# Kernel tuning notes

Measured on AMD Instinct MI355X. Metric: run time of the kernel, lower is better.

The kernel has to match this reference:

```python
import jax, jax.numpy as jnp
import numpy as np

N_EMBD = 512
N_HEAD = 8


def setup_inputs() -> dict:
    key = jax.random.key(0)
    k_x, k_aw, k_ab, k_pw, k_pb = jax.random.split(key, 5)
    B, T, E = 4, 2048, N_EMBD
    s = 1.0 / np.sqrt(E)
    return {
        "x": jax.random.normal(k_x, (B, T, E), dtype=jnp.float32),
        # torch Linear weight is [out, in]; store transposed for x @ W
        "c_attn_w": jax.random.uniform(k_aw, (E, 3 * E), jnp.float32, -s, s),
        "c_attn_b": jax.random.uniform(k_ab, (3 * E,), jnp.float32, -s, s),
        "c_proj_w": jax.random.uniform(k_pw, (E, E), jnp.float32, -s, s),
        "c_proj_b": jax.random.uniform(k_pb, (E,), jnp.float32, -s, s),
    }


def reference(x, c_attn_w, c_attn_b, c_proj_w, c_proj_b):
    B, T, E = x.shape
    H = N_HEAD
    D = E // H
    qkv = x @ c_attn_w + c_attn_b                      # [B,T,3E]
    q, k, v = jnp.split(qkv, 3, axis=2)
    # [B,T,E] -> [B,H,T,D]
    q = q.reshape(B, T, H, D).transpose(0, 2, 1, 3)
    k = k.reshape(B, T, H, D).transpose(0, 2, 1, 3)
    v = v.reshape(B, T, H, D).transpose(0, 2, 1, 3)
    scale = 1.0 / np.sqrt(D).astype(np.float32)
    scores = jnp.einsum("bhqd,bhkd->bhqk", q, k) * scale
    causal = jnp.tril(jnp.ones((T, T), dtype=bool))    # [T,T]
    scores = jnp.where(causal, scores, -jnp.inf)
    attn = jax.nn.softmax(scores, axis=-1)             # [B,H,T,T]
    y = jnp.einsum("bhqk,bhkd->bhqd", attn, v)         # [B,H,T,D]
    y = y.transpose(0, 2, 1, 3).reshape(B, T, E)
    return y @ c_proj_w + c_proj_b
```

## Files before the change

kernel.cpp:

```cpp
#include <hip/hip_runtime.h>
#include <math.h>

#define N_EMBD 512
#define N_HEAD 8
#define SEQ_T  2048
#define BATCH  4
#define QKV_LD 1536

typedef __attribute__((ext_vector_type(8))) short bf16x8;
typedef __attribute__((ext_vector_type(4))) float f32x4;

#define CL 0.18033688f

__device__ __forceinline__ unsigned short f2bf(float f) {
    union { float f; unsigned int u; } x; x.f = f;
    return (unsigned short)((x.u + 0x7FFFu + ((x.u >> 16) & 1u)) >> 16);
}
__device__ __forceinline__ unsigned pack_trunc(float a, float b) {
    union { float f; unsigned u; } x, y; x.f = a; y.f = b;
    return __builtin_amdgcn_perm(y.u, x.u, 0x07060302u);
}
__device__ __forceinline__ bf16x8 scale_frag(bf16x8 v, float c) {
    bf16x8 r;
    #pragma unroll
    for (int i = 0; i < 8; ++i) {
        union { unsigned u; float f; } x;
        x.u = ((unsigned)(unsigned short)v[i]) << 16;
        r[i] = (short)f2bf(x.f * c);
    }
    return r;
}

__device__ __forceinline__ void gl_lds16(const void* g, void* s) {
    __builtin_amdgcn_global_load_lds(
        (const __attribute__((address_space(1))) void*)g,
        (__attribute__((address_space(3))) void*)s, 16, 0, 0);
}

__global__ __launch_bounds__(256) void prep(
    const float* __restrict__ x,  unsigned short* __restrict__ x_bf,
    const float* __restrict__ w1, unsigned short* __restrict__ w1t,
    const float* __restrict__ w2, unsigned short* __restrict__ w2t)
{
    __shared__ float t[32][33];
    const int bx = blockIdx.x, tid = threadIdx.x;
    if (bx < 2048) {
        const int i = bx * 256 + tid;
        const float4 a = ((const float4*)x)[i * 2 + 0];
        const float4 b = ((const float4*)x)[i * 2 + 1];
        union { unsigned short u[8]; uint4 v; } r;
        r.u[0]=f2bf(a.x); r.u[1]=f2bf(a.y); r.u[2]=f2bf(a.z); r.u[3]=f2bf(a.w);
        r.u[4]=f2bf(b.x); r.u[5]=f2bf(b.y); r.u[6]=f2bf(b.z); r.u[7]=f2bf(b.w);
        ((uint4*)x_bf)[i] = r.v;
        return;
    }
    const float* W; unsigned short* Wt; int N, tt;
    if (bx < 2816) { tt = bx - 2048; W = w1; Wt = w1t; N = 1536; }
    else           { tt = bx - 2816; W = w2; Wt = w2t; N = 512; }
    const int nb = (bx < 2816) ? 48 : 16;
    const int n0 = (tt % nb) * 32, k0 = (tt / nb) * 32;
    const int tx = tid & 31, ty = tid >> 5;
    #pragma unroll
    for (int i = 0; i < 4; ++i)
        t[ty + i * 8][tx] = W[(size_t)(k0 + ty + i * 8) * N + n0 + tx];
    __syncthreads();
    #pragma unroll
    for (int i = 0; i < 4; ++i)
        Wt[(size_t)(n0 + ty + i * 8) * 512 + k0 + tx] = f2bf(t[tx][ty + i * 8]);
}

template <int BM, int BN, bool BF16_OUT>
__global__ __launch_bounds__(256) void gemm_mfma(
    const unsigned short* __restrict__ A,
    const unsigned short* __restrict__ Bt,
    const float* __restrict__ bias,
    void* __restrict__ C, int N, int K)
{
    constexpr int WMT = BM / 32, WNT = BN / 32;
    constexpr int NIT_A = BM / 64, NIT_B = BN / 64;
    __shared__ unsigned short As[2][BM * 32];
    __shared__ unsigned short Bs[2][BN * 32];

    const int tid  = threadIdx.x;
    const int wave = tid >> 6, lane = tid & 63;
    const int low  = lane & 15, quad = lane >> 4;
    const int wm   = (wave & 1) * (BM / 2), wn = (wave >> 1) * (BN / 2);
    const int row0 = blockIdx.y * BM, col0 = blockIdx.x * BN;

    const unsigned short* pa[NIT_A]; int da[NIT_A];
    #pragma unroll
    for (int i = 0; i < NIT_A; ++i) {
        const int p = wave * BM + i * 64 + lane;
        const int m = p >> 2, o = p & 3;
        const int q = o ^ ((m >> 1) & 3);
        pa[i] = A + (size_t)(row0 + m) * K + q * 8;
        da[i] = (wave * BM + i * 64) * 8;
    }
    const unsigned short* pb[NIT_B]; int db[NIT_B];
    #pragma unroll
    for (int i = 0; i < NIT_B; ++i) {
        const int p = wave * BN + i * 64 + lane;
        const int m = p >> 2, o = p & 3;
        const int q = o ^ ((m >> 1) & 3);
        pb[i] = Bt + (size_t)(col0 + m) * K + q * 8;
        db[i] = (wave * BN + i * 64) * 8;
    }

    f32x4 acc[WMT][WNT];
    #pragma unroll
    for (int i = 0; i < WMT; ++i)
        #pragma unroll
        for (int j = 0; j < WNT; ++j) acc[i][j] = (f32x4){0.f, 0.f, 0.f, 0.f};

    #pragma unroll
    for (int i = 0; i < NIT_A; ++i) gl_lds16(pa[i], &As[0][da[i]]);
    #pragma unroll
    for (int i = 0; i < NIT_B; ++i) gl_lds16(pb[i], &Bs[0][db[i]]);
    __syncthreads();

    const int NIT = K >> 5;
    for (int it = 0; it < NIT; ++it) {
        const int cur = it & 1;
        if (it + 1 < NIT) {
            const int ko = (it + 1) * 32;
            #pragma unroll
            for (int i = 0; i < NIT_A; ++i) gl_lds16(pa[i] + ko, &As[cur ^ 1][da[i]]);
            #pragma unroll
            for (int i = 0; i < NIT_B; ++i) gl_lds16(pb[i] + ko, &Bs[cur ^ 1][db[i]]);
        }
        const int swz = (low >> 1) & 3;
        bf16x8 af[WMT], bfr[WNT];
        #pragma unroll
        for (int t = 0; t < WMT; ++t)
            af[t] = *(const bf16x8*)&As[cur][(wm + t * 16 + low) * 32 + ((quad ^ swz) * 8)];
        #pragma unroll
        for (int t = 0; t < WNT; ++t)
            bfr[t] = *(const bf16x8*)&Bs[cur][(wn + t * 16 + low) * 32 + ((quad ^ swz) * 8)];
        #pragma unroll
        for (int i = 0; i < WMT; ++i)
            #pragma unroll
            for (int j = 0; j < WNT; ++j)
                acc[i][j] = __builtin_amdgcn_mfma_f32_16x16x32_bf16(
                    af[i], bfr[j], acc[i][j], 0, 0, 0);
        __syncthreads();
    }

    float bv[WNT];
    #pragma unroll
    for (int j = 0; j < WNT; ++j) bv[j] = bias[col0 + wn + j * 16 + low];
    #pragma unroll
    for (int i = 0; i < WMT; ++i)
        #pragma unroll
        for (int r = 0; r < 4; ++r) {
            const size_t row = row0 + wm + i * 16 + quad * 4 + r;
            #pragma unroll
            for (int j = 0; j < WNT; ++j) {
                const int col = col0 + wn + j * 16 + low;
                const float v = acc[i][j][r] + bv[j];
                if (BF16_OUT)
                    ((unsigned short*)C)[row * N + col] = f2bf(v);
                else
                    ((float*)C)[row * N + col] = v;
            }
        }
}

template <bool MASK>
__device__ __forceinline__ void tile_step(
    const bf16x8 kf[4][2], const bf16x8 qf0, const bf16x8 qf1,
    int thr, int quad, int low, unsigned short* ps)
{
    f32x4 s[4];
    #pragma unroll
    for (int st = 0; st < 4; ++st) {
        f32x4 a = (f32x4){0.f, 0.f, 0.f, 0.f};
        a = __builtin_amdgcn_mfma_f32_16x16x32_bf16(kf[st][0], qf0, a, 0, 0, 0);
        a = __builtin_amdgcn_mfma_f32_16x16x32_bf16(kf[st][1], qf1, a, 0, 0, 0);
        s[st] = a;
    }
    #pragma unroll
    for (int st = 0; st < 4; ++st) {
        float p[4];
        #pragma unroll
        for (int r = 0; r < 4; ++r) {
            float v = s[st][r];
            if (MASK) v = (st * 16 + r <= thr) ? v : -1e30f;
            p[r] = __builtin_amdgcn_exp2f(v);
        }
        uint2 pk;
        pk.x = pack_trunc(p[0], p[1]);
        pk.y = pack_trunc(p[2], p[3]);
        *(uint2*)&ps[low * 72 + st * 16 + quad * 4] = pk;
    }
}

__device__ __forceinline__ void pv_step(
    const bf16x8 vf[4][2], const unsigned short* ps, int quad, int low,
    f32x4* o, f32x4& lacc, const bf16x8 ones)
{
    const bf16x8 p0 = *(const bf16x8*)&ps[low * 72 + quad * 8];
    const bf16x8 p1 = *(const bf16x8*)&ps[low * 72 + quad * 8 + 32];
    #pragma unroll
    for (int t = 0; t < 4; ++t) {
        o[t] = __builtin_amdgcn_mfma_f32_16x16x32_bf16(p0, vf[t][0], o[t], 0, 0, 0);
        o[t] = __builtin_amdgcn_mfma_f32_16x16x32_bf16(p1, vf[t][1], o[t], 0, 0, 0);
    }
    lacc = __builtin_amdgcn_mfma_f32_16x16x32_bf16(p0, ones, lacc, 0, 0, 0);
    lacc = __builtin_amdgcn_mfma_f32_16x16x32_bf16(p1, ones, lacc, 0, 0, 0);
}

__global__ __launch_bounds__(256) void attn_mfma(
    const unsigned short* __restrict__ qkv,
    unsigned short* __restrict__ y)
{
    const int bh  = blockIdx.y;
    const int b   = bh >> 3, h = bh & 7;
    const int pa  = blockIdx.x;
    const int qA0 = pa * 64;
    const int qB0 = (31 - pa) * 64;
    const int nA  = pa + 1, nB = 32 - pa;
    const int tid = threadIdx.x;
    const int wave = tid >> 6, lane = tid & 63;
    const int low  = lane & 15, quad = lane >> 4;

    __shared__ unsigned short Ks[2][64 * 64];
    __shared__ unsigned short Vt[2][64 * 64];
    __shared__ unsigned short PsA[4][16 * 72];
    __shared__ unsigned short PsB[4][16 * 72];

    const size_t base = (size_t)b * SEQ_T * QKV_LD + h * 64;
    const unsigned short* qp = qkv + base;
    const unsigned short* kp = qkv + base + 512;
    const unsigned short* vp = qkv + base + 1024;

    const int qmyA = qA0 + wave * 16 + low;
    const int qmyB = qB0 + wave * 16 + low;

    const bf16x8 qfA0 = scale_frag(*(const bf16x8*)(qp + (size_t)qmyA * QKV_LD + quad * 8), CL);
    const bf16x8 qfA1 = scale_frag(*(const bf16x8*)(qp + (size_t)qmyA * QKV_LD + quad * 8 + 32), CL);
    const bf16x8 qfB0 = scale_frag(*(const bf16x8*)(qp + (size_t)qmyB * QKV_LD + quad * 8), CL);
    const bf16x8 qfB1 = scale_frag(*(const bf16x8*)(qp + (size_t)qmyB * QKV_LD + quad * 8 + 32), CL);

    bf16x8 ones;
    #pragma unroll
    for (int i = 0; i < 8; ++i) ones[i] = (short)0x3F80;

    const int d0 = wave * 8;
    unsigned short* psA = &PsA[wave][0];
    unsigned short* psB = &PsB[wave][0];

    bf16x8 vr0 = *(const bf16x8*)(vp + (size_t)lane * QKV_LD + d0);
    bf16x8 vr1 = *(const bf16x8*)(vp + (size_t)lane * QKV_LD + d0 + 32);
    {
        #pragma unroll
        for (int ii = 0; ii < 2; ++ii) {
            const int row = wave * 16 + ii * 8 + (lane >> 3);
            const int o   = (lane & 7) ^ (lane >> 3);
            gl_lds16(kp + (size_t)row * QKV_LD + o * 8, &Ks[0][(wave * 2 + ii) * 512]);
        }
        #pragma unroll
        for (int ii = 0; ii < 8; ++ii) {
            const int po = ((lane >> 3) ^ ii) * 8 + (lane & 7);
            Vt[0][((d0 + ii) << 6) + po]      = (unsigned short)vr0[ii];
            Vt[0][((d0 + 32 + ii) << 6) + po] = (unsigned short)vr1[ii];
        }
        if (nB > 1) {
            vr0 = *(const bf16x8*)(vp + (size_t)(64 + lane) * QKV_LD + d0);
            vr1 = *(const bf16x8*)(vp + (size_t)(64 + lane) * QKV_LD + d0 + 32);
        }
    }
    __syncthreads();

    f32x4 oA[4], oB[4], lA, lB;
    #pragma unroll
    for (int t = 0; t < 4; ++t) {
        oA[t] = (f32x4){0.f, 0.f, 0.f, 0.f};
        oB[t] = (f32x4){0.f, 0.f, 0.f, 0.f};
    }
    lA = (f32x4){0.f, 0.f, 0.f, 0.f};
    lB = (f32x4){0.f, 0.f, 0.f, 0.f};

    for (int kc = 0; kc < nB; ++kc) {
        const int cur = kc & 1;
        unsigned short* ksc = &Ks[cur][0];
        unsigned short* vtc = &Vt[cur][0];

        if (kc + 1 < nB) {
            const int key1 = (kc + 1) * 64;
            #pragma unroll
            for (int ii = 0; ii < 2; ++ii) {
                const int row = wave * 16 + ii * 8 + (lane >> 3);
                const int o   = (lane & 7) ^ (lane >> 3);
                gl_lds16(kp + (size_t)(key1 + row) * QKV_LD + o * 8,
                         &Ks[cur ^ 1][(wave * 2 + ii) * 512]);
            }
            unsigned short* vtn = &Vt[cur ^ 1][0];
            #pragma unroll
            for (int ii = 0; ii < 8; ++ii) {
                const int po = ((lane >> 3) ^ ii) * 8 + (lane & 7);
                vtn[((d0 + ii) << 6) + po]      = (unsigned short)vr0[ii];
                vtn[((d0 + 32 + ii) << 6) + po] = (unsigned short)vr1[ii];
            }
        }
        if (kc + 2 < nB) {
            const int key2 = (kc + 2) * 64;
            vr0 = *(const bf16x8*)(vp + (size_t)(key2 + lane) * QKV_LD + d0);
            vr1 = *(const bf16x8*)(vp + (size_t)(key2 + lane) * QKV_LD + d0 + 32);
        }

        const int key0 = kc * 64;
        bf16x8 kf[4][2];
        #pragma unroll
        for (int t = 0; t < 4; ++t)
            #pragma unroll
            for (int i = 0; i < 2; ++i)
                kf[t][i] = *(const bf16x8*)
                    &ksc[((t * 16 + low) << 6) + (((quad + 4 * i) ^ (low & 7)) << 3)];

        if (kc < nA) {
            if (kc == nA - 1)
                tile_step<true >(kf, qfA0, qfA1, qmyA - key0 - quad * 4, quad, low, psA);
            else
                tile_step<false>(kf, qfA0, qfA1, 0, quad, low, psA);
        }
        if (kc == nB - 1)
            tile_step<true >(kf, qfB0, qfB1, qmyB - key0 - quad * 4, quad, low, psB);
        else
            tile_step<false>(kf, qfB0, qfB1, 0, quad, low, psB);

        asm volatile("" ::: "memory");

        bf16x8 vf[4][2];
        #pragma unroll
        for (int t = 0; t < 4; ++t)
            #pragma unroll
            for (int i = 0; i < 2; ++i)
                vf[t][i] = *(const bf16x8*)
                    &vtc[((t * 16 + low) << 6) + (((quad + 4 * i) ^ (low & 7)) << 3)];

        if (kc < nA) pv_step(vf, psA, quad, low, oA, lA, ones);
        pv_step(vf, psB, quad, low, oB, lB, ones);
        __syncthreads();
    }

    #pragma unroll
    for (int r = 0; r < 4; ++r) {
        const float rlA = 1.f / lA[r];
        const int qrow = qA0 + wave * 16 + quad * 4 + r;
        unsigned short* yp = y + (size_t)(b * SEQ_T + qrow) * N_EMBD + h * 64 + low;
        #pragma unroll
        for (int t = 0; t < 4; ++t) yp[16 * t] = f2bf(oA[t][r] * rlA);
    }
    #pragma unroll
    for (int r = 0; r < 4; ++r) {
        const float rlB = 1.f / lB[r];
        const int qrow = qB0 + wave * 16 + quad * 4 + r;
        unsigned short* yp = y + (size_t)(b * SEQ_T + qrow) * N_EMBD + h * 64 + low;
        #pragma unroll
        for (int t = 0; t < 4; ++t) yp[16 * t] = f2bf(oB[t][r] * rlB);
    }
}

extern "C" void kernel_launch(void* const* d_in, const int* in_sizes, int n_in,
                              void* d_out, int out_size, void* d_ws, size_t ws_size,
                              hipStream_t stream)
{
    const float* x      = (const float*)d_in[0];
    const float* attn_w = (const float*)d_in[1];
    const float* attn_b = (const float*)d_in[2];
    const float* proj_w = (const float*)d_in[3];
    const float* proj_b = (const float*)d_in[4];
    float*       out    = (float*)d_out;

    char* ws = (char*)d_ws;
    unsigned short* qkv_bf = (unsigned short*)(ws);
    unsigned short* y_bf   = (unsigned short*)(ws + 25165824);
    unsigned short* x_bf   = (unsigned short*)(ws + 33554432);
    unsigned short* w1t    = (unsigned short*)(ws + 41943040);
    unsigned short* w2t    = (unsigned short*)(ws + 43515904);

    prep<<<3072, 256, 0, stream>>>(x, x_bf, attn_w, w1t, proj_w, w2t);

    gemm_mfma<128, 128, true><<<dim3(12, 64), 256, 0, stream>>>(
        x_bf, w1t, attn_b, qkv_bf, QKV_LD, N_EMBD);

    attn_mfma<<<dim3(16, BATCH * N_HEAD), 256, 0, stream>>>(qkv_bf, y_bf);

    gemm_mfma<64, 128, false><<<dim3(4, 128), 256, 0, stream>>>(
        y_bf, w2t, proj_b, out, N_EMBD, N_EMBD);
}
```

Before: 158.5 us.

## Restructure causal attention into flat work-item stream with register-prefetched K/V

The attention kernel drops the shared-key loop, where the A and B query tiles both consume each K/V chunk. It now runs a flat list of 33 work items (A chunks then B chunks), each a single QK/PV tile. Work items are processed two per iteration, with K and V prefetched into registers two items ahead and stored to padded LDS (72-element K rows instead of swizzling). This gives a uniform per-item cost and overlaps global loads with compute. The trade-off is that K/V chunks shared by A and B are now loaded twice, and the larger Ps buffer uses more LDS. The GEMM loop also moves its barrier to the top of each iteration.

```diff
diff --git a/kernel.cpp b/kernel.cpp
--- a/kernel.cpp
+++ b/kernel.cpp
@@ -116,11 +116,11 @@
     for (int i = 0; i < NIT_A; ++i) gl_lds16(pa[i], &As[0][da[i]]);
     #pragma unroll
     for (int i = 0; i < NIT_B; ++i) gl_lds16(pb[i], &Bs[0][db[i]]);
-    __syncthreads();
 
     const int NIT = K >> 5;
     for (int it = 0; it < NIT; ++it) {
         const int cur = it & 1;
+        __syncthreads();
         if (it + 1 < NIT) {
             const int ko = (it + 1) * 32;
             #pragma unroll
@@ -142,7 +142,6 @@
             for (int j = 0; j < WNT; ++j)
                 acc[i][j] = __builtin_amdgcn_mfma_f32_16x16x32_bf16(
                     af[i], bfr[j], acc[i][j], 0, 0, 0);
-        __syncthreads();
     }
 
     float bv[WNT];
@@ -209,6 +208,30 @@
     lacc = __builtin_amdgcn_mfma_f32_16x16x32_bf16(p1, ones, lacc, 0, 0, 0);
 }
 
+template <bool MASK>
+__device__ __forceinline__ void do_item(
+    const unsigned short* ksb, const unsigned short* vtb, unsigned short* ps,
+    const bf16x8 qf0, const bf16x8 qf1, int thr, int quad, int low,
+    f32x4 (&o)[4], f32x4& l, const bf16x8 ones)
+{
+    bf16x8 kf[4][2];
+    #pragma unroll
+    for (int t = 0; t < 4; ++t)
+        #pragma unroll
+        for (int i = 0; i < 2; ++i)
+            kf[t][i] = *(const bf16x8*)&ksb[(t * 16 + low) * 72 + (quad + 4 * i) * 8];
+    tile_step<MASK>(kf, qf0, qf1, thr, quad, low, ps);
+    asm volatile("" ::: "memory");
+    bf16x8 vf[4][2];
+    #pragma unroll
+    for (int t = 0; t < 4; ++t)
+        #pragma unroll
+        for (int i = 0; i < 2; ++i)
+            vf[t][i] = *(const bf16x8*)
+                &vtb[((t * 16 + low) << 6) + (((quad + 4 * i) ^ (low & 7)) << 3)];
+    pv_step(vf, ps, quad, low, o, l, ones);
+}
+
 __global__ __launch_bounds__(256) void attn_mfma(
     const unsigned short* __restrict__ qkv,
     unsigned short* __restrict__ y)
@@ -218,15 +241,14 @@
     const int pa  = blockIdx.x;
     const int qA0 = pa * 64;
     const int qB0 = (31 - pa) * 64;
-    const int nA  = pa + 1, nB = 32 - pa;
+    const int nA  = pa + 1;
     const int tid = threadIdx.x;
     const int wave = tid >> 6, lane = tid & 63;
     const int low  = lane & 15, quad = lane >> 4;
 
-    __shared__ unsigned short Ks[2][64 * 64];
+    __shared__ unsigned short Ks[2][64 * 72];
     __shared__ unsigned short Vt[2][64 * 64];
-    __shared__ unsigned short PsA[4][16 * 72];
-    __shared__ unsigned short PsB[4][16 * 72];
+    __shared__ unsigned short Ps[2][4][16 * 72];
 
     const size_t base = (size_t)b * SEQ_T * QKV_LD + h * 64;
     const unsigned short* qp = qkv + base;
@@ -245,32 +267,6 @@
     #pragma unroll
     for (int i = 0; i < 8; ++i) ones[i] = (short)0x3F80;
 
-    const int d0 = wave * 8;
-    unsigned short* psA = &PsA[wave][0];
-    unsigned short* psB = &PsB[wave][0];
-
-    bf16x8 vr0 = *(const bf16x8*)(vp + (size_t)lane * QKV_LD + d0);
-    bf16x8 vr1 = *(const bf16x8*)(vp + (size_t)lane * QKV_LD + d0 + 32);
-    {
-        #pragma unroll
-        for (int ii = 0; ii < 2; ++ii) {
-            const int row = wave * 16 + ii * 8 + (lane >> 3);
-            const int o   = (lane & 7) ^ (lane >> 3);
-            gl_lds16(kp + (size_t)row * QKV_LD + o * 8, &Ks[0][(wave * 2 + ii) * 512]);
-        }
-        #pragma unroll
-        for (int ii = 0; ii < 8; ++ii) {
-            const int po = ((lane >> 3) ^ ii) * 8 + (lane & 7);
-            Vt[0][((d0 + ii) << 6) + po]      = (unsigned short)vr0[ii];
-            Vt[0][((d0 + 32 + ii) << 6) + po] = (unsigned short)vr1[ii];
-        }
-        if (nB > 1) {
-            vr0 = *(const bf16x8*)(vp + (size_t)(64 + lane) * QKV_LD + d0);
-            vr1 = *(const bf16x8*)(vp + (size_t)(64 + lane) * QKV_LD + d0 + 32);
-        }
-    }
-    __syncthreads();
-
     f32x4 oA[4], oB[4], lA, lB;
     #pragma unroll
     for (int t = 0; t < 4; ++t) {
@@ -280,68 +276,93 @@
     lA = (f32x4){0.f, 0.f, 0.f, 0.f};
     lB = (f32x4){0.f, 0.f, 0.f, 0.f};
 
-    for (int kc = 0; kc < nB; ++kc) {
-        const int cur = kc & 1;
-        unsigned short* ksc = &Ks[cur][0];
-        unsigned short* vtc = &Vt[cur][0];
-
-        if (kc + 1 < nB) {
-            const int key1 = (kc + 1) * 64;
-            #pragma unroll
-            for (int ii = 0; ii < 2; ++ii) {
-                const int row = wave * 16 + ii * 8 + (lane >> 3);
-                const int o   = (lane & 7) ^ (lane >> 3);
-                gl_lds16(kp + (size_t)(key1 + row) * QKV_LD + o * 8,
-                         &Ks[cur ^ 1][(wave * 2 + ii) * 512]);
-            }
-            unsigned short* vtn = &Vt[cur ^ 1][0];
+    #define ITEM_KC(g) (((g) < nA) ? (g) : ((g) - nA))
+
+    bf16x8 k0a, k0b, v0a, v0b, k1a, k1b, v1a, v1b;
+    {
+        const size_t r0 = (size_t)(ITEM_KC(0) * 64 + lane) * QKV_LD;
+        k0a = *(const bf16x8*)(kp + r0 + wave * 16);
+        k0b = *(const bf16x8*)(kp + r0 + wave * 16 + 8);
+        v0a = *(const bf16x8*)(vp + r0 + wave * 8);
+        v0b = *(const bf16x8*)(vp + r0 + wave * 8 + 32);
+        const size_t r1 = (size_t)(ITEM_KC(1) * 64 + lane) * QKV_LD;
+        k1a = *(const bf16x8*)(kp + r1 + wave * 16);
+        k1b = *(const bf16x8*)(kp + r1 + wave * 16 + 8);
+        v1a = *(const bf16x8*)(vp + r1 + wave * 8);
+        v1b = *(const bf16x8*)(vp + r1 + wave * 8 + 32);
+    }
+
+    const int d0 = wave * 8;
+    for (int i = 0; i < 17; ++i) {
+        const int g0 = 2 * i, g1 = 2 * i + 1;
+
+        __syncthreads();
+
+        *(bf16x8*)&Ks[0][lane * 72 + wave * 16]     = k0a;
+        *(bf16x8*)&Ks[0][lane * 72 + wave * 16 + 8] = k0b;
+        #pragma unroll
+        for (int ii = 0; ii < 8; ++ii) {
+            const int po = ((lane >> 3) ^ ii) * 8 + (lane & 7);
+            Vt[0][((d0 + ii) << 6) + po]      = (unsigned short)v0a[ii];
+            Vt[0][((d0 + 32 + ii) << 6) + po] = (unsigned short)v0b[ii];
+        }
+        if (g1 <= 32) {
+            *(bf16x8*)&Ks[1][lane * 72 + wave * 16]     = k1a;
+            *(bf16x8*)&Ks[1][lane * 72 + wave * 16 + 8] = k1b;
             #pragma unroll
             for (int ii = 0; ii < 8; ++ii) {
                 const int po = ((lane >> 3) ^ ii) * 8 + (lane & 7);
-                vtn[((d0 + ii) << 6) + po]      = (unsigned short)vr0[ii];
-                vtn[((d0 + 32 + ii) << 6) + po] = (unsigned short)vr1[ii];
+                Vt[1][((d0 + ii) << 6) + po]      = (unsigned short)v1a[ii];
+                Vt[1][((d0 + 32 + ii) << 6) + po] = (unsigned short)v1b[ii];
             }
         }
-        if (kc + 2 < nB) {
-            const int key2 = (kc + 2) * 64;
-            vr0 = *(const bf16x8*)(vp + (size_t)(key2 + lane) * QKV_LD + d0);
-            vr1 = *(const bf16x8*)(vp + (size_t)(key2 + lane) * QKV_LD + d0 + 32);
-        }
-
-        const int key0 = kc * 64;
-        bf16x8 kf[4][2];
-        #pragma unroll
-        for (int t = 0; t < 4; ++t)
-            #pragma unroll
-            for (int i = 0; i < 2; ++i)
-                kf[t][i] = *(const bf16x8*)
-                    &ksc[((t * 16 + low) << 6) + (((quad + 4 * i) ^ (low & 7)) << 3)];
-
-        if (kc < nA) {
-            if (kc == nA - 1)
-                tile_step<true >(kf, qfA0, qfA1, qmyA - key0 - quad * 4, quad, low, psA);
-            else
-                tile_step<false>(kf, qfA0, qfA1, 0, quad, low, psA);
-        }
-        if (kc == nB - 1)
-            tile_step<true >(kf, qfB0, qfB1, qmyB - key0 - quad * 4, quad, low, psB);
-        else
-            tile_step<false>(kf, qfB0, qfB1, 0, quad, low, psB);
-
-        asm volatile("" ::: "memory");
-
-        bf16x8 vf[4][2];
-        #pragma unroll
-        for (int t = 0; t < 4; ++t)
-            #pragma unroll
-            for (int i = 0; i < 2; ++i)
-                vf[t][i] = *(const bf16x8*)
-                    &vtc[((t * 16 + low) << 6) + (((quad + 4 * i) ^ (low & 7)) << 3)];
-
-        if (kc < nA) pv_step(vf, psA, quad, low, oA, lA, ones);
-        pv_step(vf, psB, quad, low, oB, lB, ones);
         __syncthreads();
-    }
+
+        if (g0 + 2 <= 32) {
+            const size_t r = (size_t)(ITEM_KC(g0 + 2) * 64 + lane) * QKV_LD;
+            k0a = *(const bf16x8*)(kp + r + wave * 16);
+            k0b = *(const bf16x8*)(kp + r + wave * 16 + 8);
+            v0a = *(const bf16x8*)(vp + r + wave * 8);
+            v0b = *(const bf16x8*)(vp + r + wave * 8 + 32);
+        }
+        if (g1 + 2 <= 32) {
+            const size_t r = (size_t)(ITEM_KC(g1 + 2) * 64 + lane) * QKV_LD;
+            k1a = *(const bf16x8*)(kp + r + wave * 16);
+            k1b = *(const bf16x8*)(kp + r + wave * 16 + 8);
+            v1a = *(const bf16x8*)(vp + r + wave * 8);
+            v1b = *(const bf16x8*)(vp + r + wave * 8 + 32);
+        }
+
+        {
+            const int kc = ITEM_KC(g0);
+            const bool isA = g0 < nA;
+            const bool msk = (g0 == nA - 1) || (g0 == 32);
+            const int qmy = isA ? qmyA : qmyB;
+            const int thr = qmy - kc * 64 - quad * 4;
+            if (isA) {
+                if (msk) do_item<true >(&Ks[0][0], &Vt[0][0], &Ps[0][wave][0], qfA0, qfA1, thr, quad, low, oA, lA, ones);
+                else     do_item<false>(&Ks[0][0], &Vt[0][0], &Ps[0][wave][0], qfA0, qfA1, thr, quad, low, oA, lA, ones);
+            } else {
+                if (msk) do_item<true >(&Ks[0][0], &Vt[0][0], &Ps[0][wave][0], qfB0, qfB1, thr, quad, low, oB, lB, ones);
+                else     do_item<false>(&Ks[0][0], &Vt[0][0], &Ps[0][wave][0], qfB0, qfB1, thr, quad, low, oB, lB, ones);
+            }
+        }
+        if (g1 <= 32) {
+            const int kc = ITEM_KC(g1);
+            const bool isA = g1 < nA;
+            const bool msk = (g1 == nA - 1) || (g1 == 32);
+            const int qmy = isA ? qmyA : qmyB;
+            const int thr = qmy - kc * 64 - quad * 4;
+            if (isA) {
+                if (msk) do_item<true >(&Ks[1][0], &Vt[1][0], &Ps[1][wave][0], qfA0, qfA1, thr, quad, low, oA, lA, ones);
+                else     do_item<false>(&Ks[1][0], &Vt[1][0], &Ps[1][wave][0], qfA0, qfA1, thr, quad, low, oA, lA, ones);
+            } else {
+                if (msk) do_item<true >(&Ks[1][0], &Vt[1][0], &Ps[1][wave][0], qfB0, qfB1, thr, quad, low, oB, lB, ones);
+                else     do_item<false>(&Ks[1][0], &Vt[1][0], &Ps[1][wave][0], qfB0, qfB1, thr, quad, low, oB, lB, ones);
+            }
+        }
+    }
+    #undef ITEM_KC
 
     #pragma unroll
     for (int r = 0; r < 4; ++r) {
```

After: 171.6 us. +8.3%, slower.

## Fuse fp32-to-bf16 conversion of x into QKV GEMM with register-staged loads

Applied to the files above, without the earlier changes.

Drops the separate x-to-bf16 pass from the prep kernel. The QKV GEMM now reads fp32 x directly and converts it to bf16 by truncation while loading, which removes a full write and re-read of the bf16 copy of x. Both GEMMs switch from async global-to-LDS double buffering to register prefetch with a single LDS buffer and two barriers per iteration. That costs extra synchronisation and may overlap global latency less well. Truncation in place of round-to-nearest also slightly changes numerics.

```diff
diff --git a/kernel.cpp b/kernel.cpp
--- a/kernel.cpp
+++ b/kernel.cpp
@@ -38,26 +38,14 @@
 }
 
 __global__ __launch_bounds__(256) void prep(
-    const float* __restrict__ x,  unsigned short* __restrict__ x_bf,
     const float* __restrict__ w1, unsigned short* __restrict__ w1t,
     const float* __restrict__ w2, unsigned short* __restrict__ w2t)
 {
     __shared__ float t[32][33];
     const int bx = blockIdx.x, tid = threadIdx.x;
-    if (bx < 2048) {
-        const int i = bx * 256 + tid;
-        const float4 a = ((const float4*)x)[i * 2 + 0];
-        const float4 b = ((const float4*)x)[i * 2 + 1];
-        union { unsigned short u[8]; uint4 v; } r;
-        r.u[0]=f2bf(a.x); r.u[1]=f2bf(a.y); r.u[2]=f2bf(a.z); r.u[3]=f2bf(a.w);
-        r.u[4]=f2bf(b.x); r.u[5]=f2bf(b.y); r.u[6]=f2bf(b.z); r.u[7]=f2bf(b.w);
-        ((uint4*)x_bf)[i] = r.v;
-        return;
-    }
-    const float* W; unsigned short* Wt; int N, tt;
-    if (bx < 2816) { tt = bx - 2048; W = w1; Wt = w1t; N = 1536; }
-    else           { tt = bx - 2816; W = w2; Wt = w2t; N = 512; }
-    const int nb = (bx < 2816) ? 48 : 16;
+    const float* W; unsigned short* Wt; int N, tt, nb;
+    if (bx < 768) { tt = bx;       W = w1; Wt = w1t; N = 1536; nb = 48; }
+    else          { tt = bx - 768; W = w2; Wt = w2t; N = 512;  nb = 16; }
     const int n0 = (tt % nb) * 32, k0 = (tt / nb) * 32;
     const int tx = tid & 31, ty = tid >> 5;
     #pragma unroll
@@ -69,17 +57,17 @@
         Wt[(size_t)(n0 + ty + i * 8) * 512 + k0 + tx] = f2bf(t[tx][ty + i * 8]);
 }
 
-template <int BM, int BN, bool BF16_OUT>
+template <int BM, int BN, bool CVT_A, bool BF16_OUT>
 __global__ __launch_bounds__(256) void gemm_mfma(
-    const unsigned short* __restrict__ A,
+    const void* __restrict__ Asrc,
     const unsigned short* __restrict__ Bt,
     const float* __restrict__ bias,
     void* __restrict__ C, int N, int K)
 {
     constexpr int WMT = BM / 32, WNT = BN / 32;
-    constexpr int NIT_A = BM / 64, NIT_B = BN / 64;
-    __shared__ unsigned short As[2][BM * 32];
-    __shared__ unsigned short Bs[2][BN * 32];
+    constexpr int SA = (BM * 4) / 256, SB = (BN * 4) / 256;
+    __shared__ unsigned short As[BM * 32];
+    __shared__ unsigned short Bs[BN * 32];
 
     const int tid  = threadIdx.x;
     const int wave = tid >> 6, lane = tid & 63;
@@ -87,23 +75,21 @@
     const int wm   = (wave & 1) * (BM / 2), wn = (wave >> 1) * (BN / 2);
     const int row0 = blockIdx.y * BM, col0 = blockIdx.x * BN;
 
-    const unsigned short* pa[NIT_A]; int da[NIT_A];
-    #pragma unroll
-    for (int i = 0; i < NIT_A; ++i) {
-        const int p = wave * BM + i * 64 + lane;
-        const int m = p >> 2, o = p & 3;
-        const int q = o ^ ((m >> 1) & 3);
-        pa[i] = A + (size_t)(row0 + m) * K + q * 8;
-        da[i] = (wave * BM + i * 64) * 8;
-    }
-    const unsigned short* pb[NIT_B]; int db[NIT_B];
-    #pragma unroll
-    for (int i = 0; i < NIT_B; ++i) {
-        const int p = wave * BN + i * 64 + lane;
-        const int m = p >> 2, o = p & 3;
-        const int q = o ^ ((m >> 1) & 3);
-        pb[i] = Bt + (size_t)(col0 + m) * K + q * 8;
-        db[i] = (wave * BN + i * 64) * 8;
+    size_t a_src[SA]; int a_dst[SA];
+    #pragma unroll
+    for (int s = 0; s < SA; ++s) {
+        const int p = tid + 256 * s;
+        const int m = p >> 2, o = p & 3, q = o ^ ((m >> 1) & 3);
+        a_src[s] = (size_t)(row0 + m) * K + q * 8;
+        a_dst[s] = m * 32 + o * 8;
+    }
+    size_t b_src[SB]; int b_dst[SB];
+    #pragma unroll
+    for (int s = 0; s < SB; ++s) {
+        const int p = tid + 256 * s;
+        const int m = p >> 2, o = p & 3, q = o ^ ((m >> 1) & 3);
+        b_src[s] = (size_t)(col0 + m) * K + q * 8;
+        b_dst[s] = m * 32 + o * 8;
     }
 
     f32x4 acc[WMT][WNT];
@@ -112,37 +98,68 @@
         #pragma unroll
         for (int j = 0; j < WNT; ++j) acc[i][j] = (f32x4){0.f, 0.f, 0.f, 0.f};
 
-    #pragma unroll
-    for (int i = 0; i < NIT_A; ++i) gl_lds16(pa[i], &As[0][da[i]]);
-    #pragma unroll
-    for (int i = 0; i < NIT_B; ++i) gl_lds16(pb[i], &Bs[0][db[i]]);
-    __syncthreads();
+    bf16x8 ar[SA], br[SB];
+    const float*          af32 = (const float*)Asrc;
+    const unsigned short* a16  = (const unsigned short*)Asrc;
+
+    #pragma unroll
+    for (int s = 0; s < SA; ++s) {
+        if (CVT_A) {
+            const float4 f0 = *(const float4*)(af32 + a_src[s]);
+            const float4 f1 = *(const float4*)(af32 + a_src[s] + 4);
+            union { uint4 v; bf16x8 h; } u;
+            u.v.x = pack_trunc(f0.x, f0.y); u.v.y = pack_trunc(f0.z, f0.w);
+            u.v.z = pack_trunc(f1.x, f1.y); u.v.w = pack_trunc(f1.z, f1.w);
+            ar[s] = u.h;
+        } else {
+            ar[s] = *(const bf16x8*)(a16 + a_src[s]);
+        }
+    }
+    #pragma unroll
+    for (int s = 0; s < SB; ++s) br[s] = *(const bf16x8*)(Bt + b_src[s]);
 
     const int NIT = K >> 5;
     for (int it = 0; it < NIT; ++it) {
-        const int cur = it & 1;
+        __syncthreads();
+        #pragma unroll
+        for (int s = 0; s < SA; ++s) *(bf16x8*)&As[a_dst[s]] = ar[s];
+        #pragma unroll
+        for (int s = 0; s < SB; ++s) *(bf16x8*)&Bs[b_dst[s]] = br[s];
+        __syncthreads();
+
         if (it + 1 < NIT) {
             const int ko = (it + 1) * 32;
             #pragma unroll
-            for (int i = 0; i < NIT_A; ++i) gl_lds16(pa[i] + ko, &As[cur ^ 1][da[i]]);
-            #pragma unroll
-            for (int i = 0; i < NIT_B; ++i) gl_lds16(pb[i] + ko, &Bs[cur ^ 1][db[i]]);
-        }
+            for (int s = 0; s < SA; ++s) {
+                if (CVT_A) {
+                    const float4 f0 = *(const float4*)(af32 + a_src[s] + ko);
+                    const float4 f1 = *(const float4*)(af32 + a_src[s] + ko + 4);
+                    union { uint4 v; bf16x8 h; } u;
+                    u.v.x = pack_trunc(f0.x, f0.y); u.v.y = pack_trunc(f0.z, f0.w);
+                    u.v.z = pack_trunc(f1.x, f1.y); u.v.w = pack_trunc(f1.z, f1.w);
+                    ar[s] = u.h;
+                } else {
+                    ar[s] = *(const bf16x8*)(a16 + a_src[s] + ko);
+                }
+            }
+            #pragma unroll
+            for (int s = 0; s < SB; ++s) br[s] = *(const bf16x8*)(Bt + b_src[s] + ko);
+        }
+
         const int swz = (low >> 1) & 3;
         bf16x8 af[WMT], bfr[WNT];
         #pragma unroll
         for (int t = 0; t < WMT; ++t)
-            af[t] = *(const bf16x8*)&As[cur][(wm + t * 16 + low) * 32 + ((quad ^ swz) * 8)];
+            af[t] = *(const bf16x8*)&As[(wm + t * 16 + low) * 32 + ((quad ^ swz) * 8)];
         #pragma unroll
         for (int t = 0; t < WNT; ++t)
-            bfr[t] = *(const bf16x8*)&Bs[cur][(wn + t * 16 + low) * 32 + ((quad ^ swz) * 8)];
+            bfr[t] = *(const bf16x8*)&Bs[(wn + t * 16 + low) * 32 + ((quad ^ swz) * 8)];
         #pragma unroll
         for (int i = 0; i < WMT; ++i)
             #pragma unroll
             for (int j = 0; j < WNT; ++j)
                 acc[i][j] = __builtin_amdgcn_mfma_f32_16x16x32_bf16(
                     af[i], bfr[j], acc[i][j], 0, 0, 0);
-        __syncthreads();
     }
 
     float bv[WNT];
@@ -375,17 +392,16 @@
     char* ws = (char*)d_ws;
     unsigned short* qkv_bf = (unsigned short*)(ws);
     unsigned short* y_bf   = (unsigned short*)(ws + 25165824);
-    unsigned short* x_bf   = (unsigned short*)(ws + 33554432);
-    unsigned short* w1t    = (unsigned short*)(ws + 41943040);
-    unsigned short* w2t    = (unsigned short*)(ws + 43515904);
-
-    prep<<<3072, 256, 0, stream>>>(x, x_bf, attn_w, w1t, proj_w, w2t);
-
-    gemm_mfma<128, 128, true><<<dim3(12, 64), 256, 0, stream>>>(
-        x_bf, w1t, attn_b, qkv_bf, QKV_LD, N_EMBD);
+    unsigned short* w1t    = (unsigned short*)(ws + 33554432);
+    unsigned short* w2t    = (unsigned short*)(ws + 35127296);
+
+    prep<<<1024, 256, 0, stream>>>(attn_w, w1t, proj_w, w2t);
+
+    gemm_mfma<128, 128, true, true><<<dim3(12, 64), 256, 0, stream>>>(
+        x, w1t, attn_b, qkv_bf, QKV_LD, N_EMBD);
 
     attn_mfma<<<dim3(16, BATCH * N_HEAD), 256, 0, stream>>>(qkv_bf, y_bf);
 
-    gemm_mfma<64, 128, false><<<dim3(4, 128), 256, 0, stream>>>(
+    gemm_mfma<64, 128, false, false><<<dim3(4, 128), 256, 0, stream>>>(
         y_bf, w2t, proj_b, out, N_EMBD, N_EMBD);
 }
```

After: 159.7 us. No clear change (+0.8%).
